# Performance work log

Measured on AMD Instinct MI355X. Metric: run time of the kernel, lower is better.

## Reference

```python
import jax, jax.numpy as jnp
import numpy as np

B, T, D, H = 8, 1024, 1024, 16
DK = D // H


def setup_inputs() -> dict:
    key = jax.random.key(0)
    ks = jax.random.split(key, 12)
    inp = {
        'query': jax.random.normal(ks[0], (B, T, D), dtype=jnp.float32),
        'key': jax.random.normal(ks[1], (B, T, D), dtype=jnp.float32),
        'value': jax.random.normal(ks[2], (B, T, D), dtype=jnp.float32),
        'mask': jnp.ones((1, 1, T, T), dtype=jnp.float32),
        # Dense(d_model) params: kernel [D, D] + bias [D]
        'Wq': jax.random.normal(ks[3], (D, D), dtype=jnp.float32) * 0.02,
        'bq': jnp.zeros((D,), dtype=jnp.float32),
        'Wk': jax.random.normal(ks[4], (D, D), dtype=jnp.float32) * 0.02,
        'bk': jnp.zeros((D,), dtype=jnp.float32),
        'Wv': jax.random.normal(ks[5], (D, D), dtype=jnp.float32) * 0.02,
        'bv': jnp.zeros((D,), dtype=jnp.float32),
        'Wo': jax.random.normal(ks[6], (D, D), dtype=jnp.float32) * 0.02,
        'bo': jnp.zeros((D,), dtype=jnp.float32),
    }
    return inp


def _split_heads(x):
    # [B, T, D] -> [B, H, T, DK]
    b, t, d = x.shape
    return x.reshape(b, t, H, DK).transpose(0, 2, 1, 3)


def reference(query, key, value, mask, Wq, bq, Wk, bk, Wv, bv, Wo, bo):
    q = _split_heads(query @ Wq + bq)   # [B,H,T,DK]
    k = _split_heads(key @ Wk + bk)
    v = _split_heads(value @ Wv + bv)
    # NOTE: original code scales by rsqrt(seq_len) (tf.shape(query)[2] after
    # split_heads), NOT rsqrt(d_k). We reproduce that quirk faithfully.
    scale = jax.lax.rsqrt(jnp.float32(q.shape[2]))
    w = jnp.einsum('bhtd,bhsd->bhts', q, k) * scale  # [B,H,T,T]
    w = w * mask + (-1e9) * (1.0 - mask)
    attn = jax.nn.softmax(w, axis=-1)  # dropout is identity at inference
    x = jnp.einsum('bhts,bhsd->bhtd', attn, v)
    x = x.transpose(0, 2, 1, 3).reshape(query.shape[0], query.shape[1], D)
    return x @ Wo + bo
```

## Files before the change

### kernel.cpp

```cpp
#include <hip/hip_runtime.h>
#include <math.h>


typedef __attribute__((ext_vector_type(8))) short bf16x8;
typedef __attribute__((ext_vector_type(4))) float f32x4;

#define GCAST(p) ((const __attribute__((address_space(1))) void*)(const void*)(p))
#define LCAST(p) ((__attribute__((address_space(3))) void*)(p))

__device__ __forceinline__ short f2bf(float f) {
  union { float f; unsigned u; } c; c.f = f;
  unsigned r = c.u + 0x7fffu + ((c.u >> 16) & 1u);
  return (short)(r >> 16);
}
__device__ __forceinline__ unsigned pk_trunc(float lo, float hi) {
  return __builtin_amdgcn_perm(__float_as_uint(hi), __float_as_uint(lo), 0x07060302u);
}

__global__ __launch_bounds__(256) void cvt_all(
    const float* __restrict__ qf, const float* __restrict__ kf,
    const float* __restrict__ vf, short* __restrict__ dq,
    short* __restrict__ dk, short* __restrict__ dv,
    const float* __restrict__ W0, const float* __restrict__ W1,
    const float* __restrict__ W2, short* __restrict__ T0,
    short* __restrict__ T1, short* __restrict__ T2) {
  __shared__ short tile[64][72];
  const int bx = blockIdx.x, tid = threadIdx.x;
  if (bx < 12288) {
    const int t = bx >> 12;
    const float* s = t == 0 ? qf : (t == 1 ? kf : vf);
    short* d = t == 0 ? dq : (t == 1 ? dk : dv);
    size_t i = ((size_t)(bx & 4095) * 256 + tid) * 8;
    float4 a = *(const float4*)&s[i];
    float4 b = *(const float4*)&s[i + 4];
    bf16x8 o = {f2bf(a.x), f2bf(a.y), f2bf(a.z), f2bf(a.w),
                f2bf(b.x), f2bf(b.y), f2bf(b.z), f2bf(b.w)};
    *(bf16x8*)&d[i] = o;
  } else {
    const int w = bx - 12288;
    const int z = w >> 8, wb = w & 255;
    const float* W = z == 0 ? W0 : (z == 1 ? W1 : W2);
    short* Wt = z == 0 ? T0 : (z == 1 ? T1 : T2);
    const int n0 = (wb & 15) * 64, k0 = (wb >> 4) * 64;
#pragma unroll
    for (int i = 0; i < 4; ++i) {
      int k = (tid >> 4) + i * 16;
      int n4 = (tid & 15) * 4;
      float4 ww = *(const float4*)&W[(size_t)(k0 + k) * 1024 + n0 + n4];
      tile[k][n4 + 0] = f2bf(ww.x);
      tile[k][n4 + 1] = f2bf(ww.y);
      tile[k][n4 + 2] = f2bf(ww.z);
      tile[k][n4 + 3] = f2bf(ww.w);
    }
    __syncthreads();
#pragma unroll
    for (int i = 0; i < 2; ++i) {
      int n = (tid >> 3) + i * 32;
      int k8 = (tid & 7) * 8;
      bf16x8 v;
#pragma unroll
      for (int j = 0; j < 8; ++j) v[j] = tile[k8 + j][n];
      *(bf16x8*)&Wt[(size_t)(n0 + n) * 1024 + k0 + k8] = v;
    }
  }
}

__global__ __launch_bounds__(256) void cvt_w3(const float* __restrict__ W0,
                                              const float* __restrict__ W1,
                                              const float* __restrict__ W2,
                                              short* __restrict__ D0,
                                              short* __restrict__ D1,
                                              short* __restrict__ D2) {
  const int z = blockIdx.z;
  const float* W = z == 0 ? W0 : (z == 1 ? W1 : W2);
  short* Wt = z == 0 ? D0 : (z == 1 ? D1 : D2);
  const int tid = threadIdx.x;
  const int n0 = blockIdx.x * 64, k0 = blockIdx.y * 64;
  __shared__ short tile[64][72];
#pragma unroll
  for (int i = 0; i < 4; ++i) {
    int k = (tid >> 4) + i * 16;
    int n4 = (tid & 15) * 4;
    float4 w = *(const float4*)&W[(size_t)(k0 + k) * 1024 + n0 + n4];
    tile[k][n4 + 0] = f2bf(w.x);
    tile[k][n4 + 1] = f2bf(w.y);
    tile[k][n4 + 2] = f2bf(w.z);
    tile[k][n4 + 3] = f2bf(w.w);
  }
  __syncthreads();
#pragma unroll
  for (int i = 0; i < 2; ++i) {
    int n = (tid >> 3) + i * 32;
    int k8 = (tid & 7) * 8;
    bf16x8 v;
#pragma unroll
    for (int j = 0; j < 8; ++j) v[j] = tile[k8 + j][n];
    *(bf16x8*)&Wt[(size_t)(n0 + n) * 1024 + k0 + k8] = v;
  }
}

template <int OUT>
__global__ __launch_bounds__(512, 2) void gemm8p(
    const short* __restrict__ Aa, const short* __restrict__ Ab,
    const short* __restrict__ Ba, const short* __restrict__ Bb,
    const float* __restrict__ ca, const float* __restrict__ cb,
    void* __restrict__ oa, void* __restrict__ ob) {
  const int z = blockIdx.z;
  const short* A = z ? Ab : Aa;
  const short* Bt = z ? Bb : Ba;
  const float* bias = z ? cb : ca;
  void* outp = z ? ob : oa;

  __shared__ __align__(16) short As[2][256][64];
  __shared__ __align__(16) short Bs[2][256][64];
  short* AsF = &As[0][0][0];
  short* BsF = &Bs[0][0][0];

  const int tid = threadIdx.x, lane = tid & 63, wave = tid >> 6;
  const int mrow = lane & 15, quad = lane >> 4;
  const int wm = wave >> 2, wn = wave & 3;
  const int m0 = blockIdx.x * 256, n0 = blockIdx.y * 256;
  const int ax = (mrow & 7) << 3;

  const int idx0 = tid, idx1 = 512 + tid;
  const int r0s = idx0 >> 3, r1s = idx1 >> 3;
  const int c0s = (((idx0 & 7) ^ (r0s & 7)) * 8);
  const int c1s = (((idx1 & 7) ^ (r1s & 7)) * 8);

  const short* Ag = A + (size_t)m0 * 1024;
  const short* Bg = Bt + (size_t)n0 * 1024;

  f32x4 acc[8][4];
#pragma unroll
  for (int i = 0; i < 8; ++i)
#pragma unroll
    for (int j = 0; j < 4; ++j) acc[i][j] = f32x4{0.f, 0.f, 0.f, 0.f};

  float bias_r[4];
#pragma unroll
  for (int nc = 0; nc < 4; ++nc) bias_r[nc] = bias[n0 + wn * 64 + nc * 16 + mrow];

#define STG(GP, LB, bd, h, kt)                                               \
  __builtin_amdgcn_global_load_lds(                                          \
      GCAST((GP) + (size_t)((h)*128 + r0s) * 1024 + (kt)*64 + c0s),          \
      LCAST((LB) + (bd)*16384 + (h)*8192 + idx0 * 8), 16, 0, 0);             \
  __builtin_amdgcn_global_load_lds(                                          \
      GCAST((GP) + (size_t)((h)*128 + r1s) * 1024 + (kt)*64 + c1s),          \
      LCAST((LB) + (bd)*16384 + (h)*8192 + idx1 * 8), 16, 0, 0)

#define RDA(d, bd, mr, kh)                                                   \
  d = *(const bf16x8*)(AsF + (bd)*16384 + (wm * 128 + (mr)*16 + mrow) * 64 + \
                       (((kh)*32 + quad * 8) ^ ax))
#define RDB(d, bd, nc, kh)                                                   \
  d = *(const bf16x8*)(BsF + (bd)*16384 + (wn * 64 + (nc)*16 + mrow) * 64 +  \
                       (((kh)*32 + quad * 8) ^ ax))

#define MM(q, nc)                                                            \
  acc[2*(q)][nc] = __builtin_amdgcn_mfma_f32_16x16x32_bf16(                  \
      a00, bfr[nc][0], acc[2*(q)][nc], 0, 0, 0);                             \
  acc[2*(q)][nc] = __builtin_amdgcn_mfma_f32_16x16x32_bf16(                  \
      a01, bfr[nc][1], acc[2*(q)][nc], 0, 0, 0);                             \
  acc[2*(q)+1][nc] = __builtin_amdgcn_mfma_f32_16x16x32_bf16(                \
      a10, bfr[nc][0], acc[2*(q)+1][nc], 0, 0, 0);                           \
  acc[2*(q)+1][nc] = __builtin_amdgcn_mfma_f32_16x16x32_bf16(                \
      a11, bfr[nc][1], acc[2*(q)+1][nc], 0, 0, 0)

#define PH(bd, q, VM)                                                        \
  {                                                                          \
    bf16x8 a00, a01, a10, a11;                                               \
    RDA(a00, bd, 2 * (q), 0);                                                \
    RDA(a01, bd, 2 * (q), 1);                                                \
    RDA(a10, bd, 2 * (q) + 1, 0);                                            \
    RDA(a11, bd, 2 * (q) + 1, 1);                                            \
    if ((q) == 0) {                                                          \
      RDB(bfr[0][0], bd, 0, 0); RDB(bfr[0][1], bd, 0, 1);                    \
      RDB(bfr[1][0], bd, 1, 0); RDB(bfr[1][1], bd, 1, 1);                    \
      RDB(bfr[2][0], bd, 2, 0); RDB(bfr[2][1], bd, 2, 1);                    \
      RDB(bfr[3][0], bd, 3, 0); RDB(bfr[3][1], bd, 3, 1);                    \
    }                                                                        \
    asm volatile("" ::: "memory");                                           \
    __builtin_amdgcn_s_barrier();                                            \
    asm volatile("s_waitcnt lgkmcnt(0)" ::: "memory");                       \
    __builtin_amdgcn_s_setprio(1);                                           \
    MM(q, 0); MM(q, 1); MM(q, 2); MM(q, 3);                                  \
    __builtin_amdgcn_s_setprio(0);                                           \
    if (VM) asm volatile("s_waitcnt vmcnt(4)" ::: "memory");                 \
    asm volatile("" ::: "memory");                                           \
    __builtin_amdgcn_s_barrier();                                            \
    asm volatile("" ::: "memory");                                           \
  }

  STG(Ag, AsF, 0, 0, 0);
  STG(Ag, AsF, 0, 1, 0);
  STG(Bg, BsF, 0, 0, 0);
  STG(Bg, BsF, 0, 1, 0);
  STG(Bg, BsF, 1, 0, 1);
  STG(Bg, BsF, 1, 1, 1);
  asm volatile("s_waitcnt vmcnt(4)" ::: "memory");
  __builtin_amdgcn_s_barrier();
  asm volatile("" ::: "memory");

  bf16x8 bfr[4][2];
#pragma unroll 1
  for (int it = 0; it < 8; ++it) {
    const int t1 = 2 * it + 1;
    const int t2 = it < 7 ? 2 * it + 2 : 15;
    const int t3 = it < 7 ? 2 * it + 3 : 15;
    STG(Ag, AsF, 1, 0, t1); PH(0, 0, 0);
    STG(Ag, AsF, 1, 1, t1); PH(0, 1, 0);
    STG(Bg, BsF, 0, 0, t2); PH(0, 2, 0);
    STG(Bg, BsF, 0, 1, t2); PH(0, 3, 1);
    STG(Ag, AsF, 0, 0, t2); PH(1, 0, 0);
    STG(Ag, AsF, 0, 1, t2); PH(1, 1, 0);
    STG(Bg, BsF, 1, 0, t3); PH(1, 2, 0);
    STG(Bg, BsF, 1, 1, t3); PH(1, 3, 1);
  }
  asm volatile("s_waitcnt vmcnt(0)" ::: "memory");

#pragma unroll
  for (int mr = 0; mr < 8; ++mr) {
    const int mb = m0 + wm * 128 + mr * 16 + quad * 4;
#pragma unroll
    for (int nc = 0; nc < 4; ++nc) {
      const int n = n0 + wn * 64 + nc * 16 + mrow;
      if constexpr (OUT == 1) {
        const int bi = mb >> 10, t = mb & 1023;
        const int hh = n >> 6, dk = n & 63;
        short4 pk;
        pk.x = f2bf(acc[mr][nc][0] + bias_r[nc]);
        pk.y = f2bf(acc[mr][nc][1] + bias_r[nc]);
        pk.z = f2bf(acc[mr][nc][2] + bias_r[nc]);
        pk.w = f2bf(acc[mr][nc][3] + bias_r[nc]);
        *(short4*)&((short*)outp)[(((size_t)bi * 16 + hh) * 64 + dk) * 1024 + t] = pk;
      } else {
#pragma unroll
        for (int r = 0; r < 4; ++r) {
          const int m = mb + r;
          const float v = acc[mr][nc][r] + bias_r[nc];
          if constexpr (OUT == 0) {
            const int bi = m >> 10, t = m & 1023;
            const int hh = n >> 6, dk = n & 63;
            ((short*)outp)[(((size_t)bi * 16 + hh) * 1024 + t) * 64 + dk] = f2bf(v);
          } else {
            ((float*)outp)[(size_t)m * 1024 + n] = v;
          }
        }
      }
    }
  }
#undef STG
#undef RDA
#undef RDB
#undef MM
#undef PH
}

__global__ __launch_bounds__(256, 2) void flash_attn(const short* __restrict__ Qg,
                                                     const short* __restrict__ Kg,
                                                     const short* __restrict__ Vtg,
                                                     short* __restrict__ Xg) {
  __shared__ __align__(16) short Ks[2][2][64][32];
  __shared__ __align__(16) short Vs[2][2][64][32];
  __shared__ __align__(16) short P[4][64][72];
  const int tid = threadIdx.x, lane = tid & 63, wave = tid >> 6;
  const int mrow = lane & 15, quad = lane >> 4;
  const int bh = blockIdx.x, qb = blockIdx.y;
  const int b = bh >> 4, h = bh & 15;
  const short* Q = Qg + (size_t)bh * 65536;
  const short* K = Kg + (size_t)bh * 65536;
  const short* Vt = Vtg + (size_t)bh * 65536;
  const int q0 = qb * 256 + wave * 64;
  short* Pw = &P[wave][0][0];

  bf16x8 aq[4][2];
#pragma unroll
  for (int qs = 0; qs < 4; ++qs)
#pragma unroll
    for (int ki = 0; ki < 2; ++ki)
      aq[qs][ki] = *(const bf16x8*)&Q[(size_t)(q0 + qs * 16 + mrow) * 64 + ki * 32 + quad * 8];

  f32x4 oacc[4][4];
#pragma unroll
  for (int qs = 0; qs < 4; ++qs)
#pragma unroll
    for (int nc = 0; nc < 4; ++nc) oacc[qs][nc] = f32x4{0.f, 0.f, 0.f, 0.f};
  float lsum[4] = {0.f, 0.f, 0.f, 0.f};

  const float C = 0.03125f * 1.44269504088896f;
  const int l2 = lane >> 2;
  const int ls = (((lane & 3) ^ ((lane >> 3) & 3)) * 8);
  const int kx = ((mrow >> 1) & 3) << 3;

#define FSTG(t, bfv)                                                          \
  {                                                                           \
    const int kb_ = (t)*64;                                                   \
    _Pragma("unroll") for (int c = 0; c < 2; ++c) {                           \
      const int m_ = wave * 2 + c;                                            \
      const int ki_ = m_ >> 2, mm_ = m_ & 3;                                  \
      __builtin_amdgcn_global_load_lds(                                       \
          GCAST(K + (size_t)(kb_ + 16 * mm_ + l2) * 64 + ki_ * 32 + ls),      \
          LCAST(&Ks[bfv][ki_][16 * mm_][0] + lane * 8), 16, 0, 0);            \
      __builtin_amdgcn_global_load_lds(                                       \
          GCAST(Vt + (size_t)(16 * mm_ + l2) * 1024 + kb_ + ki_ * 32 + ls),   \
          LCAST(&Vs[bfv][ki_][16 * mm_][0] + lane * 8), 16, 0, 0);            \
    }                                                                         \
  }

  FSTG(0, 0);
#pragma unroll 2
  for (int kv = 0; kv < 16; ++kv) {
    const int bf = kv & 1;
    if (kv < 15) {
      FSTG(kv + 1, bf ^ 1);
      asm volatile("s_waitcnt vmcnt(4)" ::: "memory");
    } else {
      asm volatile("s_waitcnt vmcnt(0)" ::: "memory");
    }
    __builtin_amdgcn_s_barrier();
    asm volatile("" ::: "memory");

    bf16x8 kf[4][2];
#pragma unroll
    for (int ss = 0; ss < 4; ++ss)
#pragma unroll
      for (int ki = 0; ki < 2; ++ki)
        kf[ss][ki] = *(const bf16x8*)&Ks[bf][ki][ss * 16 + mrow][(quad * 8) ^ kx];

#pragma unroll
    for (int qs = 0; qs < 4; ++qs) {
      f32x4 sT[4];
#pragma unroll
      for (int ss = 0; ss < 4; ++ss) sT[ss] = f32x4{0.f, 0.f, 0.f, 0.f};
      __builtin_amdgcn_s_setprio(1);
#pragma unroll
      for (int ss = 0; ss < 4; ++ss)
#pragma unroll
        for (int ki = 0; ki < 2; ++ki)
          sT[ss] = __builtin_amdgcn_mfma_f32_16x16x32_bf16(kf[ss][ki], aq[qs][ki], sT[ss], 0, 0, 0);
      __builtin_amdgcn_s_setprio(0);
#pragma unroll
      for (int ss = 0; ss < 4; ++ss) {
        float p0 = __builtin_amdgcn_exp2f(sT[ss][0] * C);
        float p1 = __builtin_amdgcn_exp2f(sT[ss][1] * C);
        float p2 = __builtin_amdgcn_exp2f(sT[ss][2] * C);
        float p3 = __builtin_amdgcn_exp2f(sT[ss][3] * C);
        lsum[qs] += (p0 + p1) + (p2 + p3);
        uint2 pk = {pk_trunc(p0, p1), pk_trunc(p2, p3)};
        *(uint2*)&Pw[(qs * 16 + mrow) * 72 + ss * 16 + quad * 4] = pk;
      }
    }
#pragma unroll
    for (int ki2 = 0; ki2 < 2; ++ki2) {
      bf16x8 pa[4];
#pragma unroll
      for (int qs = 0; qs < 4; ++qs)
        pa[qs] = *(const bf16x8*)&Pw[(qs * 16 + mrow) * 72 + ki2 * 32 + quad * 8];
      __builtin_amdgcn_s_setprio(1);
#pragma unroll
      for (int nc = 0; nc < 4; ++nc) {
        bf16x8 vf = *(const bf16x8*)&Vs[bf][ki2][nc * 16 + mrow][(quad * 8) ^ kx];
#pragma unroll
        for (int qs = 0; qs < 4; ++qs)
          oacc[qs][nc] = __builtin_amdgcn_mfma_f32_16x16x32_bf16(pa[qs], vf, oacc[qs][nc], 0, 0, 0);
      }
      __builtin_amdgcn_s_setprio(0);
    }
    asm volatile("" ::: "memory");
    __builtin_amdgcn_s_barrier();
    asm volatile("" ::: "memory");
  }
#undef FSTG

  float rinv[4];
#pragma unroll
  for (int qs = 0; qs < 4; ++qs) {
    float v = lsum[qs];
    v += __shfl_xor(v, 16, 64);
    v += __shfl_xor(v, 32, 64);
    rinv[qs] = 1.0f / v;
  }
#pragma unroll
  for (int qs = 0; qs < 4; ++qs)
#pragma unroll
    for (int nc = 0; nc < 4; ++nc)
#pragma unroll
      for (int r = 0; r < 4; ++r) {
        float rr = __shfl(rinv[qs], quad * 4 + r, 64);
        int t = q0 + qs * 16 + quad * 4 + r;
        int dk = nc * 16 + mrow;
        Xg[((size_t)(b * 1024 + t)) * 1024 + h * 64 + dk] = f2bf(oacc[qs][nc][r] * rr);
      }
}

extern "C" void kernel_launch(void* const* d_in, const int* in_sizes, int n_in,
                              void* d_out, int out_size, void* d_ws, size_t ws_size,
                              hipStream_t stream) {
  const float* query = (const float*)d_in[0];
  const float* key   = (const float*)d_in[1];
  const float* value = (const float*)d_in[2];
  const float* Wq = (const float*)d_in[4];
  const float* bq = (const float*)d_in[5];
  const float* Wk = (const float*)d_in[6];
  const float* bk = (const float*)d_in[7];
  const float* Wv = (const float*)d_in[8];
  const float* bv = (const float*)d_in[9];
  const float* Wo = (const float*)d_in[10];
  const float* bo = (const float*)d_in[11];
  float* out = (float*)d_out;

  const size_t MB = 1024 * 1024;
  char* ws = (char*)d_ws;
  short* Abf_v = (short*)(ws);
  short* q_ws  = (short*)(ws);
  short* k_ws  = (short*)(ws + 16 * MB);
  short* Wtq   = (short*)(ws + 32 * MB);
  short* Wtk   = (short*)(ws + 34 * MB);
  short* Wtv   = (short*)(ws + 36 * MB);
  short* x_ws  = (short*)(ws + 32 * MB);
  short* vt_ws = (short*)(ws + 48 * MB);
  short* WoT   = q_ws;
  short* Abf_q = (short*)d_out;
  short* Abf_k = (short*)((char*)d_out + 16 * MB);

  cvt_all<<<dim3(13056), dim3(256), 0, stream>>>(query, key, value,
                                                 Abf_q, Abf_k, Abf_v,
                                                 Wq, Wk, Wv, Wtq, Wtk, Wtv);
  gemm8p<1><<<dim3(32, 4, 1), dim3(512), 0, stream>>>(Abf_v, Abf_v, Wtv, Wtv,
                                                      bv, bv, vt_ws, vt_ws);
  gemm8p<0><<<dim3(32, 4, 2), dim3(512), 0, stream>>>(Abf_q, Abf_k, Wtq, Wtk,
                                                      bq, bk, q_ws, k_ws);
  flash_attn<<<dim3(128, 4), dim3(256), 0, stream>>>(q_ws, k_ws, vt_ws, x_ws);
  cvt_w3<<<dim3(16, 16, 1), dim3(256), 0, stream>>>(Wo, Wo, Wo, WoT, WoT, WoT);
  gemm8p<2><<<dim3(32, 4, 1), dim3(512), 0, stream>>>(x_ws, x_ws, WoT, WoT,
                                                      bo, bo, (void*)out, (void*)out);
}
```

Baseline: 319.1 us.

## Fuse fp32-to-bf16 activation conversion into 128x128 projection GEMM loads

Removes the separate activation conversion pass: the QKV projection GEMM now reads fp32 inputs directly, converts them in registers with v_cvt_pk_bf16_f32, and writes them into swizzled LDS. All three projections run in one launch, and the output projection uses the same kernel. The GEMM tile drops from 256x256 with 512 threads to 128x128 with 256 threads and a simpler double-buffered K=32 loop. All four weight transposes now happen in one kernel. This saves a full fp32 read plus bf16 write/read of Q/K/V activations, but the A loads go through registers and the smaller tiles give less data reuse per block.

```diff
diff --git a/kernel.cpp b/kernel.cpp
--- a/kernel.cpp
+++ b/kernel.cpp
@@ -4,6 +4,7 @@
 
 typedef __attribute__((ext_vector_type(8))) short bf16x8;
 typedef __attribute__((ext_vector_type(4))) float f32x4;
+typedef __attribute__((ext_vector_type(4))) unsigned u32x4;
 
 #define GCAST(p) ((const __attribute__((address_space(1))) void*)(const void*)(p))
 #define LCAST(p) ((__attribute__((address_space(3))) void*)(p))
@@ -13,67 +14,23 @@
   unsigned r = c.u + 0x7fffu + ((c.u >> 16) & 1u);
   return (short)(r >> 16);
 }
+__device__ __forceinline__ unsigned cvtpk(float a, float b) {
+  unsigned r;
+  asm("v_cvt_pk_bf16_f32 %0, %1, %2" : "=v"(r) : "v"(a), "v"(b));
+  return r;
+}
 __device__ __forceinline__ unsigned pk_trunc(float lo, float hi) {
   return __builtin_amdgcn_perm(__float_as_uint(hi), __float_as_uint(lo), 0x07060302u);
 }
 
-__global__ __launch_bounds__(256) void cvt_all(
-    const float* __restrict__ qf, const float* __restrict__ kf,
-    const float* __restrict__ vf, short* __restrict__ dq,
-    short* __restrict__ dk, short* __restrict__ dv,
+__global__ __launch_bounds__(256) void cvt_w4(
     const float* __restrict__ W0, const float* __restrict__ W1,
-    const float* __restrict__ W2, short* __restrict__ T0,
-    short* __restrict__ T1, short* __restrict__ T2) {
-  __shared__ short tile[64][72];
-  const int bx = blockIdx.x, tid = threadIdx.x;
-  if (bx < 12288) {
-    const int t = bx >> 12;
-    const float* s = t == 0 ? qf : (t == 1 ? kf : vf);
-    short* d = t == 0 ? dq : (t == 1 ? dk : dv);
-    size_t i = ((size_t)(bx & 4095) * 256 + tid) * 8;
-    float4 a = *(const float4*)&s[i];
-    float4 b = *(const float4*)&s[i + 4];
-    bf16x8 o = {f2bf(a.x), f2bf(a.y), f2bf(a.z), f2bf(a.w),
-                f2bf(b.x), f2bf(b.y), f2bf(b.z), f2bf(b.w)};
-    *(bf16x8*)&d[i] = o;
-  } else {
-    const int w = bx - 12288;
-    const int z = w >> 8, wb = w & 255;
-    const float* W = z == 0 ? W0 : (z == 1 ? W1 : W2);
-    short* Wt = z == 0 ? T0 : (z == 1 ? T1 : T2);
-    const int n0 = (wb & 15) * 64, k0 = (wb >> 4) * 64;
-#pragma unroll
-    for (int i = 0; i < 4; ++i) {
-      int k = (tid >> 4) + i * 16;
-      int n4 = (tid & 15) * 4;
-      float4 ww = *(const float4*)&W[(size_t)(k0 + k) * 1024 + n0 + n4];
-      tile[k][n4 + 0] = f2bf(ww.x);
-      tile[k][n4 + 1] = f2bf(ww.y);
-      tile[k][n4 + 2] = f2bf(ww.z);
-      tile[k][n4 + 3] = f2bf(ww.w);
-    }
-    __syncthreads();
-#pragma unroll
-    for (int i = 0; i < 2; ++i) {
-      int n = (tid >> 3) + i * 32;
-      int k8 = (tid & 7) * 8;
-      bf16x8 v;
-#pragma unroll
-      for (int j = 0; j < 8; ++j) v[j] = tile[k8 + j][n];
-      *(bf16x8*)&Wt[(size_t)(n0 + n) * 1024 + k0 + k8] = v;
-    }
-  }
-}
-
-__global__ __launch_bounds__(256) void cvt_w3(const float* __restrict__ W0,
-                                              const float* __restrict__ W1,
-                                              const float* __restrict__ W2,
-                                              short* __restrict__ D0,
-                                              short* __restrict__ D1,
-                                              short* __restrict__ D2) {
+    const float* __restrict__ W2, const float* __restrict__ W3,
+    short* __restrict__ D0, short* __restrict__ D1,
+    short* __restrict__ D2, short* __restrict__ D3) {
   const int z = blockIdx.z;
-  const float* W = z == 0 ? W0 : (z == 1 ? W1 : W2);
-  short* Wt = z == 0 ? D0 : (z == 1 ? D1 : D2);
+  const float* W = z == 0 ? W0 : (z == 1 ? W1 : (z == 2 ? W2 : W3));
+  short* Wt = z == 0 ? D0 : (z == 1 ? D1 : (z == 2 ? D2 : D3));
   const int tid = threadIdx.x;
   const int n0 = blockIdx.x * 64, k0 = blockIdx.y * 64;
   __shared__ short tile[64][72];
@@ -99,40 +56,41 @@
   }
 }
 
-template <int OUT>
-__global__ __launch_bounds__(512, 2) void gemm8p(
-    const short* __restrict__ Aa, const short* __restrict__ Ab,
-    const short* __restrict__ Ba, const short* __restrict__ Bb,
-    const float* __restrict__ ca, const float* __restrict__ cb,
-    void* __restrict__ oa, void* __restrict__ ob) {
+template <int AFP32, int OUT>
+__global__ __launch_bounds__(256, 4) void gemm128(
+    const void* __restrict__ A0, const void* __restrict__ A1,
+    const void* __restrict__ A2, const short* __restrict__ B0,
+    const short* __restrict__ B1, const short* __restrict__ B2,
+    const float* __restrict__ c0, const float* __restrict__ c1,
+    const float* __restrict__ c2, void* __restrict__ o0,
+    void* __restrict__ o1, void* __restrict__ o2) {
   const int z = blockIdx.z;
-  const short* A = z ? Ab : Aa;
-  const short* Bt = z ? Bb : Ba;
-  const float* bias = z ? cb : ca;
-  void* outp = z ? ob : oa;
-
-  __shared__ __align__(16) short As[2][256][64];
-  __shared__ __align__(16) short Bs[2][256][64];
-  short* AsF = &As[0][0][0];
-  short* BsF = &Bs[0][0][0];
+  const void* Ap = z == 0 ? A0 : (z == 1 ? A1 : A2);
+  const short* Bt = z == 0 ? B0 : (z == 1 ? B1 : B2);
+  const float* bias = z == 0 ? c0 : (z == 1 ? c1 : c2);
+  void* outp = z == 0 ? o0 : (z == 1 ? o1 : o2);
+
+  __shared__ __align__(16) short As[2][128 * 32];
+  __shared__ __align__(16) short Bs[2][128 * 32];
 
   const int tid = threadIdx.x, lane = tid & 63, wave = tid >> 6;
   const int mrow = lane & 15, quad = lane >> 4;
-  const int wm = wave >> 2, wn = wave & 3;
-  const int m0 = blockIdx.x * 256, n0 = blockIdx.y * 256;
-  const int ax = (mrow & 7) << 3;
-
-  const int idx0 = tid, idx1 = 512 + tid;
-  const int r0s = idx0 >> 3, r1s = idx1 >> 3;
-  const int c0s = (((idx0 & 7) ^ (r0s & 7)) * 8);
-  const int c1s = (((idx1 & 7) ^ (r1s & 7)) * 8);
-
-  const short* Ag = A + (size_t)m0 * 1024;
+  const int wm = wave >> 1, wn = wave & 1;
+  const int n0 = blockIdx.x * 128, m0 = blockIdx.y * 128;
+  const int sx = ((mrow >> 1) & 3) << 3;
+
+  const int brow = tid >> 2;
+  const int bcol = 8 * ((tid & 3) ^ ((tid >> 3) & 3));
   const short* Bg = Bt + (size_t)n0 * 1024;
-
-  f32x4 acc[8][4];
-#pragma unroll
-  for (int i = 0; i < 8; ++i)
+  const short* Ag = AFP32 ? nullptr : (const short*)Ap + (size_t)m0 * 1024;
+  const int sr = tid >> 1, sch = tid & 1;
+  const int sx2 = (tid >> 2) & 3;
+  const float* Af32 =
+      AFP32 ? (const float*)Ap + (size_t)(m0 + sr) * 1024 + 16 * sch : nullptr;
+
+  f32x4 acc[4][4];
+#pragma unroll
+  for (int i = 0; i < 4; ++i)
 #pragma unroll
     for (int j = 0; j < 4; ++j) acc[i][j] = f32x4{0.f, 0.f, 0.f, 0.f};
 
@@ -140,119 +98,105 @@
 #pragma unroll
   for (int nc = 0; nc < 4; ++nc) bias_r[nc] = bias[n0 + wn * 64 + nc * 16 + mrow];
 
-#define STG(GP, LB, bd, h, kt)                                               \
-  __builtin_amdgcn_global_load_lds(                                          \
-      GCAST((GP) + (size_t)((h)*128 + r0s) * 1024 + (kt)*64 + c0s),          \
-      LCAST((LB) + (bd)*16384 + (h)*8192 + idx0 * 8), 16, 0, 0);             \
-  __builtin_amdgcn_global_load_lds(                                          \
-      GCAST((GP) + (size_t)((h)*128 + r1s) * 1024 + (kt)*64 + c1s),          \
-      LCAST((LB) + (bd)*16384 + (h)*8192 + idx1 * 8), 16, 0, 0)
-
-#define RDA(d, bd, mr, kh)                                                   \
-  d = *(const bf16x8*)(AsF + (bd)*16384 + (wm * 128 + (mr)*16 + mrow) * 64 + \
-                       (((kh)*32 + quad * 8) ^ ax))
-#define RDB(d, bd, nc, kh)                                                   \
-  d = *(const bf16x8*)(BsF + (bd)*16384 + (wn * 64 + (nc)*16 + mrow) * 64 +  \
-                       (((kh)*32 + quad * 8) ^ ax))
-
-#define MM(q, nc)                                                            \
-  acc[2*(q)][nc] = __builtin_amdgcn_mfma_f32_16x16x32_bf16(                  \
-      a00, bfr[nc][0], acc[2*(q)][nc], 0, 0, 0);                             \
-  acc[2*(q)][nc] = __builtin_amdgcn_mfma_f32_16x16x32_bf16(                  \
-      a01, bfr[nc][1], acc[2*(q)][nc], 0, 0, 0);                             \
-  acc[2*(q)+1][nc] = __builtin_amdgcn_mfma_f32_16x16x32_bf16(                \
-      a10, bfr[nc][0], acc[2*(q)+1][nc], 0, 0, 0);                           \
-  acc[2*(q)+1][nc] = __builtin_amdgcn_mfma_f32_16x16x32_bf16(                \
-      a11, bfr[nc][1], acc[2*(q)+1][nc], 0, 0, 0)
-
-#define PH(bd, q, VM)                                                        \
-  {                                                                          \
-    bf16x8 a00, a01, a10, a11;                                               \
-    RDA(a00, bd, 2 * (q), 0);                                                \
-    RDA(a01, bd, 2 * (q), 1);                                                \
-    RDA(a10, bd, 2 * (q) + 1, 0);                                            \
-    RDA(a11, bd, 2 * (q) + 1, 1);                                            \
-    if ((q) == 0) {                                                          \
-      RDB(bfr[0][0], bd, 0, 0); RDB(bfr[0][1], bd, 0, 1);                    \
-      RDB(bfr[1][0], bd, 1, 0); RDB(bfr[1][1], bd, 1, 1);                    \
-      RDB(bfr[2][0], bd, 2, 0); RDB(bfr[2][1], bd, 2, 1);                    \
-      RDB(bfr[3][0], bd, 3, 0); RDB(bfr[3][1], bd, 3, 1);                    \
-    }                                                                        \
-    asm volatile("" ::: "memory");                                           \
-    __builtin_amdgcn_s_barrier();                                            \
-    asm volatile("s_waitcnt lgkmcnt(0)" ::: "memory");                       \
-    __builtin_amdgcn_s_setprio(1);                                           \
-    MM(q, 0); MM(q, 1); MM(q, 2); MM(q, 3);                                  \
-    __builtin_amdgcn_s_setprio(0);                                           \
-    if (VM) asm volatile("s_waitcnt vmcnt(4)" ::: "memory");                 \
-    asm volatile("" ::: "memory");                                           \
-    __builtin_amdgcn_s_barrier();                                            \
-    asm volatile("" ::: "memory");                                           \
-  }
-
-  STG(Ag, AsF, 0, 0, 0);
-  STG(Ag, AsF, 0, 1, 0);
-  STG(Bg, BsF, 0, 0, 0);
-  STG(Bg, BsF, 0, 1, 0);
-  STG(Bg, BsF, 1, 0, 1);
-  STG(Bg, BsF, 1, 1, 1);
-  asm volatile("s_waitcnt vmcnt(4)" ::: "memory");
-  __builtin_amdgcn_s_barrier();
-  asm volatile("" ::: "memory");
-
-  bf16x8 bfr[4][2];
+#define STGB(bd, kof)                                                         \
+  _Pragma("unroll") for (int i_ = 0; i_ < 2; ++i_)                            \
+      __builtin_amdgcn_global_load_lds(                                       \
+          GCAST(Bg + (size_t)(i_ * 64 + brow) * 1024 + (kof) + bcol),         \
+          LCAST(&Bs[bd][i_ * 2048 + tid * 8]), 16, 0, 0)
+#define STGA_BF(bd, kof)                                                      \
+  _Pragma("unroll") for (int i_ = 0; i_ < 2; ++i_)                            \
+      __builtin_amdgcn_global_load_lds(                                       \
+          GCAST(Ag + (size_t)(i_ * 64 + brow) * 1024 + (kof) + bcol),         \
+          LCAST(&As[bd][i_ * 2048 + tid * 8]), 16, 0, 0)
+#define WRA_FP(bd)                                                            \
+  {                                                                           \
+    unsigned u_[8];                                                           \
+    _Pragma("unroll") for (int i_ = 0; i_ < 4; ++i_) {                        \
+      u_[2 * i_] = cvtpk(a4[i_].x, a4[i_].y);                                 \
+      u_[2 * i_ + 1] = cvtpk(a4[i_].z, a4[i_].w);                             \
+    }                                                                         \
+    short* d_ = &As[bd][sr * 32];                                             \
+    const int s0_ = (2 * sch) ^ sx2, s1_ = (2 * sch + 1) ^ sx2;               \
+    *(u32x4*)&d_[s0_ * 8] = u32x4{u_[0], u_[1], u_[2], u_[3]};                \
+    *(u32x4*)&d_[s1_ * 8] = u32x4{u_[4], u_[5], u_[6], u_[7]};                \
+  }
+
+  float4 a4[4];
+  if constexpr (AFP32) {
+#pragma unroll
+    for (int i = 0; i < 4; ++i) a4[i] = ((const float4*)Af32)[i];
+  } else {
+    STGA_BF(0, 0);
+  }
+  STGB(0, 0);
+  if constexpr (AFP32) WRA_FP(0);
+  __syncthreads();
+
 #pragma unroll 1
-  for (int it = 0; it < 8; ++it) {
-    const int t1 = 2 * it + 1;
-    const int t2 = it < 7 ? 2 * it + 2 : 15;
-    const int t3 = it < 7 ? 2 * it + 3 : 15;
-    STG(Ag, AsF, 1, 0, t1); PH(0, 0, 0);
-    STG(Ag, AsF, 1, 1, t1); PH(0, 1, 0);
-    STG(Bg, BsF, 0, 0, t2); PH(0, 2, 0);
-    STG(Bg, BsF, 0, 1, t2); PH(0, 3, 1);
-    STG(Ag, AsF, 0, 0, t2); PH(1, 0, 0);
-    STG(Ag, AsF, 0, 1, t2); PH(1, 1, 0);
-    STG(Bg, BsF, 1, 0, t3); PH(1, 2, 0);
-    STG(Bg, BsF, 1, 1, t3); PH(1, 3, 1);
-  }
-  asm volatile("s_waitcnt vmcnt(0)" ::: "memory");
-
-#pragma unroll
-  for (int mr = 0; mr < 8; ++mr) {
-    const int mb = m0 + wm * 128 + mr * 16 + quad * 4;
+  for (int it = 0; it < 32; ++it) {
+    const int cu = it & 1, nx = cu ^ 1;
+    const int kn = (it < 31 ? it + 1 : 31) * 32;
+    if constexpr (AFP32) {
+#pragma unroll
+      for (int i = 0; i < 4; ++i) a4[i] = ((const float4*)(Af32 + kn))[i];
+    } else {
+      STGA_BF(nx, kn);
+    }
+    STGB(nx, kn);
+    bf16x8 af[4], bf[4];
+#pragma unroll
+    for (int mr = 0; mr < 4; ++mr)
+      af[mr] = *(const bf16x8*)&As[cu][(wm * 64 + mr * 16 + mrow) * 32 +
+                                       ((quad << 3) ^ sx)];
+#pragma unroll
+    for (int nc = 0; nc < 4; ++nc)
+      bf[nc] = *(const bf16x8*)&Bs[cu][(wn * 64 + nc * 16 + mrow) * 32 +
+                                       ((quad << 3) ^ sx)];
+    __builtin_amdgcn_s_setprio(1);
+#pragma unroll
+    for (int mr = 0; mr < 4; ++mr)
+#pragma unroll
+      for (int nc = 0; nc < 4; ++nc)
+        acc[mr][nc] = __builtin_amdgcn_mfma_f32_16x16x32_bf16(af[mr], bf[nc],
+                                                              acc[mr][nc], 0, 0, 0);
+    __builtin_amdgcn_s_setprio(0);
+    if constexpr (AFP32) WRA_FP(nx);
+    __syncthreads();
+  }
+
+#pragma unroll
+  for (int mr = 0; mr < 4; ++mr) {
+    const int mb = m0 + wm * 64 + mr * 16 + quad * 4;
 #pragma unroll
     for (int nc = 0; nc < 4; ++nc) {
       const int n = n0 + wn * 64 + nc * 16 + mrow;
-      if constexpr (OUT == 1) {
-        const int bi = mb >> 10, t = mb & 1023;
-        const int hh = n >> 6, dk = n & 63;
-        short4 pk;
-        pk.x = f2bf(acc[mr][nc][0] + bias_r[nc]);
-        pk.y = f2bf(acc[mr][nc][1] + bias_r[nc]);
-        pk.z = f2bf(acc[mr][nc][2] + bias_r[nc]);
-        pk.w = f2bf(acc[mr][nc][3] + bias_r[nc]);
-        *(short4*)&((short*)outp)[(((size_t)bi * 16 + hh) * 64 + dk) * 1024 + t] = pk;
+      const int bi = mb >> 10, t = mb & 1023;
+      const int hh = n >> 6, dk = n & 63;
+      const bool tr = (OUT == 1) || (OUT == 3 && z == 2);
+      if constexpr (OUT == 2) {
+#pragma unroll
+        for (int r = 0; r < 4; ++r)
+          ((float*)outp)[(size_t)(mb + r) * 1024 + n] = acc[mr][nc][r] + bias_r[nc];
       } else {
-#pragma unroll
-        for (int r = 0; r < 4; ++r) {
-          const int m = mb + r;
-          const float v = acc[mr][nc][r] + bias_r[nc];
-          if constexpr (OUT == 0) {
-            const int bi = m >> 10, t = m & 1023;
-            const int hh = n >> 6, dk = n & 63;
-            ((short*)outp)[(((size_t)bi * 16 + hh) * 1024 + t) * 64 + dk] = f2bf(v);
-          } else {
-            ((float*)outp)[(size_t)m * 1024 + n] = v;
-          }
+        if (tr) {
+          short4 pk;
+          pk.x = f2bf(acc[mr][nc][0] + bias_r[nc]);
+          pk.y = f2bf(acc[mr][nc][1] + bias_r[nc]);
+          pk.z = f2bf(acc[mr][nc][2] + bias_r[nc]);
+          pk.w = f2bf(acc[mr][nc][3] + bias_r[nc]);
+          *(short4*)&((short*)outp)[(((size_t)bi * 16 + hh) * 64 + dk) * 1024 + t] = pk;
+        } else {
+#pragma unroll
+          for (int r = 0; r < 4; ++r)
+            ((short*)outp)[(((size_t)bi * 16 + hh) * 1024 + t + r) * 64 + dk] =
+                f2bf(acc[mr][nc][r] + bias_r[nc]);
         }
       }
     }
   }
-#undef STG
-#undef RDA
-#undef RDB
-#undef MM
-#undef PH
+#undef STGB
+#undef STGA_BF
+#undef WRA_FP
 }
 
 __global__ __launch_bounds__(256, 2) void flash_attn(const short* __restrict__ Qg,
@@ -410,27 +354,20 @@
 
   const size_t MB = 1024 * 1024;
   char* ws = (char*)d_ws;
-  short* Abf_v = (short*)(ws);
   short* q_ws  = (short*)(ws);
   short* k_ws  = (short*)(ws + 16 * MB);
   short* Wtq   = (short*)(ws + 32 * MB);
   short* Wtk   = (short*)(ws + 34 * MB);
   short* Wtv   = (short*)(ws + 36 * MB);
-  short* x_ws  = (short*)(ws + 32 * MB);
-  short* vt_ws = (short*)(ws + 48 * MB);
-  short* WoT   = q_ws;
-  short* Abf_q = (short*)d_out;
-  short* Abf_k = (short*)((char*)d_out + 16 * MB);
-
-  cvt_all<<<dim3(13056), dim3(256), 0, stream>>>(query, key, value,
-                                                 Abf_q, Abf_k, Abf_v,
-                                                 Wq, Wk, Wv, Wtq, Wtk, Wtv);
-  gemm8p<1><<<dim3(32, 4, 1), dim3(512), 0, stream>>>(Abf_v, Abf_v, Wtv, Wtv,
-                                                      bv, bv, vt_ws, vt_ws);
-  gemm8p<0><<<dim3(32, 4, 2), dim3(512), 0, stream>>>(Abf_q, Abf_k, Wtq, Wtk,
-                                                      bq, bk, q_ws, k_ws);
+  short* WoT   = (short*)(ws + 38 * MB);
+  short* x_ws  = (short*)(ws + 40 * MB);
+  short* vt_ws = (short*)d_out;
+
+  cvt_w4<<<dim3(16, 16, 4), dim3(256), 0, stream>>>(Wq, Wk, Wv, Wo,
+                                                    Wtq, Wtk, Wtv, WoT);
+  gemm128<1, 3><<<dim3(8, 64, 3), dim3(256), 0, stream>>>(
+      query, key, value, Wtq, Wtk, Wtv, bq, bk, bv, q_ws, k_ws, vt_ws);
   flash_attn<<<dim3(128, 4), dim3(256), 0, stream>>>(q_ws, k_ws, vt_ws, x_ws);
-  cvt_w3<<<dim3(16, 16, 1), dim3(256), 0, stream>>>(Wo, Wo, Wo, WoT, WoT, WoT);
-  gemm8p<2><<<dim3(32, 4, 1), dim3(512), 0, stream>>>(x_ws, x_ws, WoT, WoT,
-                                                      bo, bo, (void*)out, (void*)out);
-}
+  gemm128<0, 2><<<dim3(8, 64, 1), dim3(256), 0, stream>>>(
+      x_ws, x_ws, x_ws, WoT, WoT, WoT, bo, bo, bo, (void*)out, (void*)out, (void*)out);
+}
```

New measurement: 340.5 us. +6.7%, slower.
